# Kernel optimization log

Hardware: AMD Instinct MI355X
Metric: run time of the kernel (lower is better)

Reference implementation:

```python
import jax, jax.numpy as jnp
import numpy as np

C = 64   # input_channels
H = 128  # hidden_channels


def setup_inputs() -> dict:
    key = jax.random.key(0)
    ks = jax.random.split(key, 13)
    s = lambda k, shape, fan_in: jax.random.uniform(k, shape, jnp.float32, -1.0, 1.0) / np.sqrt(fan_in)
    return {
        "x": jax.random.normal(ks[0], (2, 512, C), jnp.float32),
        "Wa": s(ks[1], (C, H), C),  "ba": s(ks[2], (H,), C),
        "Wb": s(ks[3], (H, H), H), "bb": s(ks[4], (H,), H),
        "Wc1": s(ks[5], (H, H), H), "bc1": s(ks[6], (H,), H),
        "Wc2": s(ks[7], (H, H), H), "bc2": s(ks[8], (H,), H),
        "Wc3": s(ks[9], (H, H), H), "bc3": s(ks[10], (H,), H),
        "Wo": s(ks[11], (H, 1), H), "bo": s(ks[12], (1,), H),
    }


def reference(x, Wa, ba, Wb, bb, Wc1, bc1, Wc2, bc2, Wc3, bc3, Wo, bo):
    B, N, _ = x.shape
    # node MLP
    h = jax.nn.relu(jnp.einsum("bnc,ch->bnh", x, Wa) + ba)
    h = jax.nn.relu(jnp.einsum("bnh,hk->bnk", h, Wb) + bb)
    # pairwise difference: diff[b,i,j] = h[b,j] - h[b,i]  (matches x_a - x_b)
    d = h[:, None, :, :] - h[:, :, None, :]  # [B,N,N,H]
    e = jax.nn.relu(jnp.einsum("bijh,hk->bijk", d, Wc1) + bc1)
    e = jax.nn.relu(jnp.einsum("bijh,hk->bijk", e, Wc2) + bc2)
    e = jax.nn.relu(jnp.einsum("bijh,hk->bijk", e, Wc3) + bc3)
    out = jnp.einsum("bijh,ho->bijo", e, Wo) + bo  # [B,N,N,1]
    return out[..., 0]  # [B,N,N]
```

## Files before the change

### kernel.cpp

```cpp
#include <hip/hip_runtime.h>


typedef _Float16 half_t;
typedef __attribute__((ext_vector_type(2))) _Float16 f16x2;
typedef __attribute__((ext_vector_type(8))) _Float16 f16x8;
typedef __attribute__((ext_vector_type(4))) float f32x4;


__global__ __launch_bounds__(256) void prep_kernel(
    const float* __restrict__ x, const float* __restrict__ Wa, const float* __restrict__ ba,
    const float* __restrict__ Wb, const float* __restrict__ bb, const float* __restrict__ Wc1,
    const float* __restrict__ bc1, const float* __restrict__ Wc2, const float* __restrict__ Wc3,
    half_t* __restrict__ gh, half_t* __restrict__ gbh,
    half_t* __restrict__ W2T, half_t* __restrict__ W3T)
{
  const int t = threadIdx.x;
  if (blockIdx.x >= 256) {
    const int bid = blockIdx.x - 256;
    const int layer = bid >> 3, nt = bid & 7;
    const int ks = t >> 6, L = t & 63, q = L >> 4, cc = L & 15;
    const float* src = layer ? Wc3 : Wc2;
    half_t* dst = layer ? W3T : W2T;
    f16x8 v;
    #pragma unroll
    for (int e = 0; e < 8; e++)
      v[e] = (half_t)src[(32 * ks + 8 * q + e) * 128 + 16 * nt + cc];
    *(f16x8*)(dst + (nt * 4 + ks) * 512 + L * 8) = v;
    return;
  }
  __shared__ float sx[64 * 6];
  __shared__ float sh1[128 * 6];
  __shared__ float sh2[128 * 6];
  const int n0 = blockIdx.x * 4;
  const int col = t & 127, hf = t >> 7;

  sx[(t & 63) * 6 + (t >> 6)] = x[(n0 + (t >> 6)) * 64 + (t & 63)];
  __syncthreads();

  float a0 = ba[col], a1 = a0;
  #pragma unroll
  for (int cc = 0; cc < 64; cc++) {
    const float wv = Wa[cc * 128 + col];
    const float2 xv = *(const float2*)(sx + cc * 6 + hf * 2);
    a0 = fmaf(xv.x, wv, a0); a1 = fmaf(xv.y, wv, a1);
  }
  *(float2*)(sh1 + col * 6 + hf * 2) = make_float2(fmaxf(a0, 0.f), fmaxf(a1, 0.f));
  __syncthreads();

  float b0 = bb[col], b1 = b0;
  #pragma unroll
  for (int k = 0; k < 128; k++) {
    const float wv = Wb[k * 128 + col];
    const float2 hv = *(const float2*)(sh1 + k * 6 + hf * 2);
    b0 = fmaf(hv.x, wv, b0); b1 = fmaf(hv.y, wv, b1);
  }
  *(float2*)(sh2 + col * 6 + hf * 2) = make_float2(fmaxf(b0, 0.f), fmaxf(b1, 0.f));
  __syncthreads();

  float c0 = 0.f, c1 = 0.f;
  #pragma unroll
  for (int k = 0; k < 128; k++) {
    const float wv = Wc1[k * 128 + col];
    const float2 hv = *(const float2*)(sh2 + k * 6 + hf * 2);
    c0 = fmaf(hv.x, wv, c0); c1 = fmaf(hv.y, wv, c1);
  }
  const float bv = bc1[col];
  const int r0 = n0 + hf * 2;
  gh [(r0 + 0) * 128 + col] = (half_t)c0;
  gh [(r0 + 1) * 128 + col] = (half_t)c1;
  gbh[(r0 + 0) * 128 + col] = (half_t)(c0 + bv);
  gbh[(r0 + 1) * 128 + col] = (half_t)(c1 + bv);
}

static __device__ inline f16x8 relu_sub8(f16x8 a, f16x8 b) {
  f16x8 d = a - b;
  const f16x8 z = {};
  return __builtin_elementwise_max(d, z);
}

__global__ __launch_bounds__(256, 4)
void edge_kernel(
    const half_t* __restrict__ gh, const half_t* __restrict__ gbh,
    const half_t* __restrict__ W2T, const half_t* __restrict__ W3T,
    const float* __restrict__ bc2, const float* __restrict__ bc3,
    const float* __restrict__ Wo, const float* __restrict__ bo,
    float* __restrict__ out)
{
  __shared__ half_t sE[4 * 8 * 512];
  const int t = threadIdx.x, lane = t & 63, w = t >> 6;
  const int c = lane & 15, q = lane >> 4;
  const int bid = blockIdx.x;
  const int b = bid >> 9, jq = (bid >> 7) & 3, ic = bid & 127;
  const int i0 = ic * 4;
  const int j0w = jq * 128 + w * 32;

  half_t* sEw = sE + w * (8 * 512);
  const float bo0 = bo[0];
  const int packoff = ((q >> 1) * 16 + c) * 8 + (q & 1) * 4;
  const int rdoff = lane * 8;

  f16x8 gj[4][2];
  #pragma unroll
  for (int ks = 0; ks < 4; ks++)
    #pragma unroll
    for (int jt = 0; jt < 2; jt++)
      gj[ks][jt] = *(const f16x8*)(gbh + (size_t)(b * 512 + j0w + jt * 16 + c) * 128 + ks * 32 + q * 8);

  #pragma unroll 1
  for (int u = 0; u < 4; u++) {
    const int i = i0 + u;

    f16x8 e1[4][2];
    {
      f16x8 gih[4];
      #pragma unroll
      for (int ks = 0; ks < 4; ks++)
        gih[ks] = *(const f16x8*)(gh + (size_t)(b * 512 + i) * 128 + ks * 32 + q * 8);
      #pragma unroll
      for (int ks = 0; ks < 4; ks++)
        #pragma unroll
        for (int jt = 0; jt < 2; jt++)
          e1[ks][jt] = relu_sub8(gj[ks][jt], gih[ks]);
    }

    #pragma unroll 1
    for (int nt = 0; nt < 8; nt++) {
      f16x8 wf[4];
      #pragma unroll
      for (int ks = 0; ks < 4; ks++)
        wf[ks] = *(const f16x8*)(W2T + nt * 2048 + ks * 512 + rdoff);
      const f32x4 b2 = *(const f32x4*)(bc2 + nt * 16 + q * 4);
      f32x4 acc[2] = {b2, b2};
      __builtin_amdgcn_s_setprio(1);
      #pragma unroll
      for (int ks = 0; ks < 4; ks++)
        #pragma unroll
        for (int jt = 0; jt < 2; jt++)
          acc[jt] = __builtin_amdgcn_mfma_f32_16x16x32_f16(wf[ks], e1[ks][jt], acc[jt], 0, 0, 0);
      __builtin_amdgcn_s_setprio(0);
      const int po = ((nt >> 1) * 512) + packoff + (nt & 1) * 256;
      #pragma unroll
      for (int jt = 0; jt < 2; jt++) {
        const f32x4 v = acc[jt];
        f16x2 h01, h23;
        h01[0] = (half_t)fmaxf(v[0], 0.f); h01[1] = (half_t)fmaxf(v[1], 0.f);
        h23[0] = (half_t)fmaxf(v[2], 0.f); h23[1] = (half_t)fmaxf(v[3], 0.f);
        uint2 uv;
        uv.x = __builtin_bit_cast(unsigned int, h01);
        uv.y = __builtin_bit_cast(unsigned int, h23);
        *(uint2*)(sEw + jt * 2048 + po) = uv;
      }
    }

    f16x8 be[4][2];
    #pragma unroll
    for (int ks3 = 0; ks3 < 4; ks3++)
      #pragma unroll
      for (int jt = 0; jt < 2; jt++)
        be[ks3][jt] = *(const f16x8*)(sEw + (jt * 4 + ks3) * 512 + rdoff);

    float p[2] = {0.f, 0.f};
    #pragma unroll 1
    for (int nt = 0; nt < 8; nt++) {
      f16x8 wf[4];
      #pragma unroll
      for (int ks3 = 0; ks3 < 4; ks3++)
        wf[ks3] = *(const f16x8*)(W3T + nt * 2048 + ks3 * 512 + rdoff);
      const f32x4 b3 = *(const f32x4*)(bc3 + nt * 16 + q * 4);
      f32x4 acc[2] = {b3, b3};
      __builtin_amdgcn_s_setprio(1);
      #pragma unroll
      for (int ks3 = 0; ks3 < 4; ks3++)
        #pragma unroll
        for (int jt = 0; jt < 2; jt++)
          acc[jt] = __builtin_amdgcn_mfma_f32_16x16x32_f16(wf[ks3], be[ks3][jt], acc[jt], 0, 0, 0);
      __builtin_amdgcn_s_setprio(0);
      const f32x4 wo = *(const f32x4*)(Wo + nt * 16 + q * 4);
      #pragma unroll
      for (int jt = 0; jt < 2; jt++)
        #pragma unroll
        for (int r = 0; r < 4; r++)
          p[jt] = fmaf(fmaxf(acc[jt][r], 0.f), wo[r], p[jt]);
    }

    #pragma unroll
    for (int jt = 0; jt < 2; jt++) {
      p[jt] += __shfl_xor(p[jt], 16, 64);
      p[jt] += __shfl_xor(p[jt], 32, 64);
    }
    if (q == 0) {
      const size_t base = ((size_t)(b * 512 + i)) * 512 + j0w;
      #pragma unroll
      for (int jt = 0; jt < 2; jt++)
        out[base + jt * 16 + c] = p[jt] + bo0;
    }
  }
}

extern "C" void kernel_launch(void* const* d_in, const int* in_sizes, int n_in,
                              void* d_out, int out_size, void* d_ws, size_t ws_size,
                              hipStream_t stream)
{
  const float* x   = (const float*)d_in[0];
  const float* Wa  = (const float*)d_in[1];
  const float* ba  = (const float*)d_in[2];
  const float* Wb  = (const float*)d_in[3];
  const float* bb  = (const float*)d_in[4];
  const float* Wc1 = (const float*)d_in[5];
  const float* bc1 = (const float*)d_in[6];
  const float* Wc2 = (const float*)d_in[7];
  const float* bc2 = (const float*)d_in[8];
  const float* Wc3 = (const float*)d_in[9];
  const float* bc3 = (const float*)d_in[10];
  const float* Wo  = (const float*)d_in[11];
  const float* bo  = (const float*)d_in[12];
  float* out = (float*)d_out;

  char* ws = (char*)d_ws;
  half_t* gh  = (half_t*)ws;
  half_t* gbh = (half_t*)(ws + 262144);
  half_t* W2T = (half_t*)(ws + 524288);
  half_t* W3T = (half_t*)(ws + 557056);

  prep_kernel<<<272, 256, 0, stream>>>(x, Wa, ba, Wb, bb, Wc1, bc1, Wc2, Wc3,
                                       gh, gbh, W2T, W3T);
  edge_kernel<<<1024, 256, 0, stream>>>(gh, gbh, W2T, W3T, bc2, bc3, Wo, bo, out);
}
```

Measured before the change: 132.6 us.

## Stage edge-MLP weights and biases in LDS with larger 512-thread blocks

Each edge block now copies the fp16 transposed Wc2/Wc3 weights and the bc2/bc3/Wo vectors into shared memory once. MFMA operands are then read from LDS instead of global/L1 on every nt iteration. Blocks double to 512 threads covering 256 j columns each, halving the grid and spreading the staging cost over more work. The nt loops are also fully unrolled. The trade-off is about 130 KB of LDS per block, which limits occupancy, plus higher register pressure from the unrolling.

```diff
diff --git a/kernel.cpp b/kernel.cpp
--- a/kernel.cpp
+++ b/kernel.cpp
@@ -78,7 +78,7 @@
   return __builtin_elementwise_max(d, z);
 }
 
-__global__ __launch_bounds__(256, 4)
+__global__ __launch_bounds__(512, 2)
 void edge_kernel(
     const half_t* __restrict__ gh, const half_t* __restrict__ gbh,
     const half_t* __restrict__ W2T, const half_t* __restrict__ W3T,
@@ -86,15 +86,28 @@
     const float* __restrict__ Wo, const float* __restrict__ bo,
     float* __restrict__ out)
 {
-  __shared__ half_t sE[4 * 8 * 512];
+  __shared__ __align__(16) half_t sW2[16384];
+  __shared__ __align__(16) half_t sW3[16384];
+  __shared__ __align__(16) float  sBf[384];
+  __shared__ __align__(16) half_t sE[8 * 4096];
+
   const int t = threadIdx.x, lane = t & 63, w = t >> 6;
   const int c = lane & 15, q = lane >> 4;
   const int bid = blockIdx.x;
-  const int b = bid >> 9, jq = (bid >> 7) & 3, ic = bid & 127;
+  const int b = bid >> 8, jh = (bid >> 7) & 1, ic = bid & 127;
   const int i0 = ic * 4;
-  const int j0w = jq * 128 + w * 32;
-
-  half_t* sEw = sE + w * (8 * 512);
+  const int j0w = jh * 256 + w * 32;
+
+  #pragma unroll
+  for (int k = 0; k < 4; k++) {
+    const int off = (k * 512 + t) * 8;
+    *(f16x8*)(sW2 + off) = *(const f16x8*)(W2T + off);
+    *(f16x8*)(sW3 + off) = *(const f16x8*)(W3T + off);
+  }
+  if (t < 384) sBf[t] = (t < 128) ? bc2[t] : ((t < 256) ? bc3[t - 128] : Wo[t - 256]);
+  __syncthreads();
+
+  half_t* sEw = sE + w * 4096;
   const float bo0 = bo[0];
   const int packoff = ((q >> 1) * 16 + c) * 8 + (q & 1) * 4;
   const int rdoff = lane * 8;
@@ -123,13 +136,13 @@
           e1[ks][jt] = relu_sub8(gj[ks][jt], gih[ks]);
     }
 
-    #pragma unroll 1
+    #pragma unroll
     for (int nt = 0; nt < 8; nt++) {
       f16x8 wf[4];
       #pragma unroll
       for (int ks = 0; ks < 4; ks++)
-        wf[ks] = *(const f16x8*)(W2T + nt * 2048 + ks * 512 + rdoff);
-      const f32x4 b2 = *(const f32x4*)(bc2 + nt * 16 + q * 4);
+        wf[ks] = *(const f16x8*)(sW2 + nt * 2048 + ks * 512 + rdoff);
+      const f32x4 b2 = *(const f32x4*)(sBf + nt * 16 + q * 4);
       f32x4 acc[2] = {b2, b2};
       __builtin_amdgcn_s_setprio(1);
       #pragma unroll
@@ -160,13 +173,13 @@
         be[ks3][jt] = *(const f16x8*)(sEw + (jt * 4 + ks3) * 512 + rdoff);
 
     float p[2] = {0.f, 0.f};
-    #pragma unroll 1
+    #pragma unroll
     for (int nt = 0; nt < 8; nt++) {
       f16x8 wf[4];
       #pragma unroll
       for (int ks3 = 0; ks3 < 4; ks3++)
-        wf[ks3] = *(const f16x8*)(W3T + nt * 2048 + ks3 * 512 + rdoff);
-      const f32x4 b3 = *(const f32x4*)(bc3 + nt * 16 + q * 4);
+        wf[ks3] = *(const f16x8*)(sW3 + nt * 2048 + ks3 * 512 + rdoff);
+      const f32x4 b3 = *(const f32x4*)(sBf + 128 + nt * 16 + q * 4);
       f32x4 acc[2] = {b3, b3};
       __builtin_amdgcn_s_setprio(1);
       #pragma unroll
@@ -175,7 +188,7 @@
         for (int jt = 0; jt < 2; jt++)
           acc[jt] = __builtin_amdgcn_mfma_f32_16x16x32_f16(wf[ks3], be[ks3][jt], acc[jt], 0, 0, 0);
       __builtin_amdgcn_s_setprio(0);
-      const f32x4 wo = *(const f32x4*)(Wo + nt * 16 + q * 4);
+      const f32x4 wo = *(const f32x4*)(sBf + 256 + nt * 16 + q * 4);
       #pragma unroll
       for (int jt = 0; jt < 2; jt++)
         #pragma unroll
@@ -224,5 +237,5 @@
 
   prep_kernel<<<272, 256, 0, stream>>>(x, Wa, ba, Wb, bb, Wc1, bc1, Wc2, Wc3,
                                        gh, gbh, W2T, W3T);
-  edge_kernel<<<1024, 256, 0, stream>>>(gh, gbh, W2T, W3T, bc2, bc3, Wo, bo, out);
-}
+  edge_kernel<<<512, 512, 0, stream>>>(gh, gbh, W2T, W3T, bc2, bc3, Wo, bo, out);
+}
```

New measurement: 118.7 us. 1.12x faster.
